# Performance work log

Measured on AMD Instinct MI355X. Metric: run time of the kernel, lower is better.

Reference implementation:

```python
import jax, jax.numpy as jnp
import numpy as np

H = 1024      # hidden_size
I = 2048      # intermediate_size
E = 32        # num_routed_experts
B, S = 4, 2048


def setup_inputs() -> dict:
    key = jax.random.key(0)
    ks = jax.random.split(key, 8)
    scale = 0.02
    inp = {
        "hidden_states": jax.random.normal(ks[0], (B, S, H), dtype=jnp.float32),
        # router gate: stored [H, E] so logits = x @ gate_w
        "gate_w": jax.random.normal(ks[1], (H, E), dtype=jnp.float32) * scale,
        # shared SwiGLU (num_shared_experts=1), weights stored [in, out]
        "shared_gate_w": jax.random.normal(ks[2], (H, I), dtype=jnp.float32) * scale,
        "shared_up_w": jax.random.normal(ks[3], (H, I), dtype=jnp.float32) * scale,
        "shared_down_w": jax.random.normal(ks[4], (I, H), dtype=jnp.float32) * scale,
        # routed grouped SwiGLU, weights stored [E, in, out] (matches GroupedLinear)
        "routed_gate_w": jax.random.normal(ks[5], (E, H, I), dtype=jnp.float32) * scale,
        "routed_up_w": jax.random.normal(ks[6], (E, H, I), dtype=jnp.float32) * scale,
        "routed_down_w": jax.random.normal(ks[7], (E, I, H), dtype=jnp.float32) * scale,
    }
    return inp


def _grouped_mm(a, w, group_sizes):
    # a: [T, in], w: [E, in, out], group_sizes: [E] int32 -> [T, out]
    return jax.lax.ragged_dot(a, w, group_sizes)


def _swiglu(x, gw, uw, dw):
    return (jax.nn.silu(x @ gw) * (x @ uw)) @ dw


def reference(hidden_states, gate_w, shared_gate_w, shared_up_w, shared_down_w,
              routed_gate_w, routed_up_w, routed_down_w):
    b, s, h = hidden_states.shape
    x = hidden_states.reshape(-1, h)                      # [T, H]

    # ---- shared expert ----
    shared_out = _swiglu(x, shared_gate_w, shared_up_w, shared_down_w)

    # ---- router: top-1 ----
    logits = x @ gate_w                                   # [T, E]
    topk_ids = jnp.argmax(logits, axis=-1)                # [T]
    topk_val = jnp.max(logits, axis=-1)                   # [T]
    scores = jax.nn.sigmoid(topk_val)[:, None]            # [T, 1]
    xs = x * scores                                       # scale tokens by router score

    # ---- dispatch: sort tokens by expert id ----
    tokens_per_expert = jnp.zeros((E,), jnp.int32).at[topk_ids].add(1)
    order = jnp.argsort(topk_ids)                         # token ids sorted by expert
    sorted_x = xs[order]                                  # [T, H]

    # ---- grouped SwiGLU experts ----
    g = _grouped_mm(sorted_x, routed_gate_w, tokens_per_expert)   # [T, I]
    u = _grouped_mm(sorted_x, routed_up_w, tokens_per_expert)     # [T, I]
    d = _grouped_mm(jax.nn.silu(g) * u, routed_down_w, tokens_per_expert)  # [T, H]

    # ---- combine: unsort back to token order ----
    inv = jnp.argsort(order)
    routed_out = d[inv]

    return (shared_out + routed_out).reshape(b, s, h)
```

## Files before the change

### kernel.cpp

```cpp
#include <hip/hip_runtime.h>
#include <stdint.h>
#include <stddef.h>

#define TOK 8192
#define H 1024
#define IDIM 2048
#define NE 32
#define BM 128
#define BN 128
#define BK 64
#define MAX_TILES 96

typedef __attribute__((ext_vector_type(8))) short short8;
typedef __attribute__((ext_vector_type(4))) float f32x4;
typedef __attribute__((ext_vector_type(4))) float float4v;
typedef __attribute__((ext_vector_type(4))) unsigned int uint4v;


__device__ __forceinline__ unsigned short f2bf(float x) {
  unsigned u = __builtin_bit_cast(unsigned, x);
  u += 0x7fffu + ((u >> 16) & 1u);
  return (unsigned short)(u >> 16);
}

__device__ __forceinline__ unsigned cvtpk(float lo, float hi) {
  unsigned r;
  asm("v_cvt_pk_bf16_f32 %0, %1, %2" : "=v"(r) : "v"(lo), "v"(hi));
  return r;
}

__device__ __forceinline__ void gll16(const void* g, void* l) {
  __builtin_amdgcn_global_load_lds(
      (const __attribute__((address_space(1))) unsigned int*)g,
      (__attribute__((address_space(3))) unsigned int*)l, 16, 0, 0);
}

__device__ __forceinline__ f32x4 mfma16(short8 a, short8 b, f32x4 c) {
  return __builtin_amdgcn_mfma_f32_16x16x32_bf16(a, b, c, 0, 0, 0);
}

__device__ __forceinline__ int wswz(int n) {
  return ((n ^ (n >> 2)) & 7) << 4;
}


__global__ __launch_bounds__(256) void router_kernel(
    const float* __restrict__ x, const float* __restrict__ gw,
    unsigned short* __restrict__ xbf, unsigned short* __restrict__ xsbf,
    int* __restrict__ expert_id, int* __restrict__ counts)
{
  __shared__ float xl[8 * H];
  __shared__ float plog[8][8][NE];
  __shared__ float sscore[8];
  const int tid = threadIdx.x;
  const long t0 = (long)blockIdx.x * 8;

  const float4v* src = (const float4v*)(x + t0 * H);
  float4v* dst = (float4v*)xl;
  #pragma unroll
  for (int i = 0; i < 8; ++i) dst[tid + i * 256] = src[tid + i * 256];
  __syncthreads();

  {
    const int e = tid & 31, c = tid >> 5;
    float acc[8] = {0, 0, 0, 0, 0, 0, 0, 0};
    const float* gp = gw + (c * 128) * NE + e;
    for (int h = 0; h < 128; ++h) {
      float g = gp[h * NE];
      const float* xr = xl + (c * 128 + h);
      #pragma unroll
      for (int tk = 0; tk < 8; ++tk) acc[tk] += xr[tk * H] * g;
    }
    #pragma unroll
    for (int tk = 0; tk < 8; ++tk) plog[c][tk][e] = acc[tk];
  }
  __syncthreads();
  {
    const int e = tid & 31, tok = tid >> 5;
    float lg = 0.f;
    #pragma unroll
    for (int c = 0; c < 8; ++c) lg += plog[c][tok][e];
    float m = lg; int be = e;
    #pragma unroll
    for (int mask = 16; mask >= 1; mask >>= 1) {
      float om = __shfl_xor(m, mask);
      int   oe = __shfl_xor(be, mask);
      if (om > m || (om == m && oe < be)) { m = om; be = oe; }
    }
    if (e == 0) {
      sscore[tok] = 1.f / (1.f + __expf(-m));
      expert_id[t0 + tok] = be;
      atomicAdd(&counts[be], 1);
    }
  }
  __syncthreads();
  {
    const float sc = sscore[tid >> 5];
    const int base = (tid >> 5) * H + (tid & 31) * 32;
    #pragma unroll
    for (int i = 0; i < 4; ++i) {
      uint4v vx, vs;
      #pragma unroll
      for (int q = 0; q < 4; ++q) {
        const float a = xl[base + i * 8 + 2 * q];
        const float b = xl[base + i * 8 + 2 * q + 1];
        vx[q] = cvtpk(a, b);
        vs[q] = cvtpk(a * sc, b * sc);
      }
      *(uint4v*)(xbf  + t0 * H + base + i * 8) = vx;
      *(uint4v*)(xsbf + t0 * H + base + i * 8) = vs;
    }
  }
}


__global__ void scan_kernel(const int* __restrict__ counts, int* __restrict__ offsets,
                            int* __restrict__ cursor, int* __restrict__ tile_e,
                            int* __restrict__ tile_p, int* __restrict__ n_tiles)
{
  if (threadIdx.x != 0) return;
  int off = 0, nt = 0;
  for (int e = 0; e < NE; ++e) {
    offsets[e] = off; cursor[e] = off;
    int cc = counts[e];
    for (int k = 0; k < cc; k += BM) { tile_e[nt] = e; tile_p[nt] = off + k; ++nt; }
    off += cc;
  }
  offsets[NE] = off;
  n_tiles[0] = nt;
}


__global__ __launch_bounds__(256) void perm_kernel(
    const int* __restrict__ expert_id, int* __restrict__ cursor, int* __restrict__ perm)
{
  int t = blockIdx.x * 256 + threadIdx.x;
  int e = expert_id[t];
  int pos = atomicAdd(&cursor[e], 1);
  perm[pos] = t;
}


template<bool ROUTED>
__global__ __launch_bounds__(256, 2) void gateup_kernel(
    const unsigned short* __restrict__ Abase,
    const float* __restrict__ WgAll, const float* __restrict__ WuAll,
    unsigned short* __restrict__ act,
    const int* __restrict__ perm, const int* __restrict__ tile_e,
    const int* __restrict__ tile_p, const int* __restrict__ offsets,
    const int* __restrict__ n_tiles)
{
  __shared__ short Alds[2][BM * BK];
  __shared__ short Glds[BN * BK];
  __shared__ short Ulds[BN * BK];

  const int tid = threadIdx.x;
  const int wave = tid >> 6, lane = tid & 63;
  const int wm = wave >> 1, wn = wave & 1;

  int row0, row_end;
  const float *Wg, *Wu;
  if constexpr (ROUTED) {
    if ((int)blockIdx.x >= *n_tiles) return;
    const int e = tile_e[blockIdx.x];
    row0 = tile_p[blockIdx.x];
    row_end = offsets[e + 1];
    Wg = WgAll + (size_t)e * H * IDIM;
    Wu = WuAll + (size_t)e * H * IDIM;
  } else {
    row0 = blockIdx.x * BM; row_end = row0 + BM;
    Wg = WgAll; Wu = WuAll;
  }
  const int n0 = blockIdx.y * BN;

  const unsigned short* asrc[4];
  int aoff[4];
  #pragma unroll
  for (int i = 0; i < 4; ++i) {
    const int r = wave * 32 + i * 8 + (lane >> 3);
    int grow;
    if constexpr (ROUTED) {
      int p = row0 + r;
      if (p >= row_end) p = row0;
      grow = perm[p];
    } else grow = row0 + r;
    const int cb = ((lane & 7) * 16) ^ ((r & 7) << 4);
    asrc[i] = Abase + (size_t)grow * H + (cb >> 1);
    aoff[i] = (wave * 32 + i * 8) * BK;
  }

  const int wq = tid >> 5;
  const int wc = tid & 31;

  f32x4 accg[4][4] = {};
  f32x4 accu[4][4] = {};
  float4v g4[8], u4[8];

  auto stageA = [&](int kt) {
    short* base = Alds[kt & 1];
    #pragma unroll
    for (int i = 0; i < 4; ++i) gll16(asrc[i] + kt * BK, base + aoff[i]);
  };
  auto loadW = [&](int kt) {
    const int k0 = kt * BK;
    #pragma unroll
    for (int r = 0; r < 8; ++r) {
      const size_t goff = (size_t)(k0 + wq * 8 + r) * IDIM + (n0 + wc * 4);
      g4[r] = *(const float4v*)(Wg + goff);
      u4[r] = *(const float4v*)(Wu + goff);
    }
  };
  auto writeW = [&]() {
    #pragma unroll
    for (int j = 0; j < 4; ++j) {
      const int n = wc * 4 + j;
      const int cb = (wq * 16) ^ wswz(n);
      uint4v pg, pu;
      pg.x = cvtpk(g4[0][j], g4[1][j]);
      pg.y = cvtpk(g4[2][j], g4[3][j]);
      pg.z = cvtpk(g4[4][j], g4[5][j]);
      pg.w = cvtpk(g4[6][j], g4[7][j]);
      pu.x = cvtpk(u4[0][j], u4[1][j]);
      pu.y = cvtpk(u4[2][j], u4[3][j]);
      pu.z = cvtpk(u4[4][j], u4[5][j]);
      pu.w = cvtpk(u4[6][j], u4[7][j]);
      *(uint4v*)((char*)Glds + n * 128 + cb) = pg;
      *(uint4v*)((char*)Ulds + n * 128 + cb) = pu;
    }
  };
  auto compute = [&](int kt) {
    const char* ab = (const char*)Alds[kt & 1];
    #pragma unroll
    for (int kk = 0; kk < 2; ++kk) {
      short8 af[4];
      #pragma unroll
      for (int m = 0; m < 4; ++m) {
        const int r = wm * 64 + m * 16 + (lane & 15);
        const int cb = (kk * 64 + ((lane >> 4) * 16)) ^ ((r & 7) << 4);
        af[m] = *(const short8*)(ab + r * 128 + cb);
      }
      #pragma unroll
      for (int nf = 0; nf < 4; ++nf) {
        const int n = wn * 64 + nf * 16 + (lane & 15);
        const int cb = (kk * 64 + ((lane >> 4) * 16)) ^ wswz(n);
        short8 bg = *(const short8*)((const char*)Glds + n * 128 + cb);
        short8 bu = *(const short8*)((const char*)Ulds + n * 128 + cb);
        #pragma unroll
        for (int m = 0; m < 4; ++m) {
          accg[m][nf] = mfma16(af[m], bg, accg[m][nf]);
          accu[m][nf] = mfma16(af[m], bu, accu[m][nf]);
        }
      }
    }
  };

  stageA(0);
  loadW(0);
  writeW();
  __syncthreads();

  #pragma unroll 1
  for (int kt = 0; kt < H / BK - 1; ++kt) {
    stageA(kt + 1);
    loadW(kt + 1);
    compute(kt);
    __syncthreads();
    writeW();
    __syncthreads();
  }
  compute(H / BK - 1);

  #pragma unroll
  for (int m = 0; m < 4; ++m)
    #pragma unroll
    for (int nf = 0; nf < 4; ++nf) {
      const int col = n0 + wn * 64 + nf * 16 + (lane & 15);
      #pragma unroll
      for (int j = 0; j < 4; ++j) {
        const int row = row0 + wm * 64 + m * 16 + ((lane >> 4) * 4) + j;
        if (ROUTED && row >= row_end) continue;
        const float g = accg[m][nf][j];
        const float u = accu[m][nf][j];
        const float v = (g / (1.f + __expf(-g))) * u;
        act[(size_t)row * IDIM + col] = f2bf(v);
      }
    }
}


template<bool ROUTED>
__global__ __launch_bounds__(256, 2) void down_kernel(
    const unsigned short* __restrict__ act,
    const float* __restrict__ WdAll,
    float* __restrict__ out,
    const int* __restrict__ perm, const int* __restrict__ tile_e,
    const int* __restrict__ tile_p, const int* __restrict__ offsets,
    const int* __restrict__ n_tiles)
{
  __shared__ short Alds[2][BM * BK];
  __shared__ short Wlds[BN * BK];

  const int tid = threadIdx.x;
  const int wave = tid >> 6, lane = tid & 63;
  const int wm = wave >> 1, wn = wave & 1;

  int row0, row_end;
  const float* Wd;
  if constexpr (ROUTED) {
    if ((int)blockIdx.x >= *n_tiles) return;
    const int e = tile_e[blockIdx.x];
    row0 = tile_p[blockIdx.x];
    row_end = offsets[e + 1];
    Wd = WdAll + (size_t)e * IDIM * H;
  } else {
    row0 = blockIdx.x * BM; row_end = row0 + BM;
    Wd = WdAll;
  }
  const int n0 = blockIdx.y * BN;

  const unsigned short* asrc[4];
  int aoff[4];
  #pragma unroll
  for (int i = 0; i < 4; ++i) {
    const int r = wave * 32 + i * 8 + (lane >> 3);
    int p = row0 + r;
    if (ROUTED && p >= row_end) p = row0;
    const int cb = ((lane & 7) * 16) ^ ((r & 7) << 4);
    asrc[i] = act + (size_t)p * IDIM + (cb >> 1);
    aoff[i] = (wave * 32 + i * 8) * BK;
  }

  const int wq = tid >> 5;
  const int wc = tid & 31;

  f32x4 acc[4][4] = {};
  float4v w4[8];

  auto stageA = [&](int kt) {
    short* base = Alds[kt & 1];
    #pragma unroll
    for (int i = 0; i < 4; ++i) gll16(asrc[i] + kt * BK, base + aoff[i]);
  };
  auto loadW = [&](int kt) {
    const int k0 = kt * BK;
    #pragma unroll
    for (int r = 0; r < 8; ++r)
      w4[r] = *(const float4v*)(Wd + (size_t)(k0 + wq * 8 + r) * H + (n0 + wc * 4));
  };
  auto writeW = [&]() {
    #pragma unroll
    for (int j = 0; j < 4; ++j) {
      const int n = wc * 4 + j;
      const int cb = (wq * 16) ^ wswz(n);
      uint4v pw;
      pw.x = cvtpk(w4[0][j], w4[1][j]);
      pw.y = cvtpk(w4[2][j], w4[3][j]);
      pw.z = cvtpk(w4[4][j], w4[5][j]);
      pw.w = cvtpk(w4[6][j], w4[7][j]);
      *(uint4v*)((char*)Wlds + n * 128 + cb) = pw;
    }
  };
  auto compute = [&](int kt) {
    const char* ab = (const char*)Alds[kt & 1];
    #pragma unroll
    for (int kk = 0; kk < 2; ++kk) {
      short8 af[4];
      #pragma unroll
      for (int m = 0; m < 4; ++m) {
        const int r = wm * 64 + m * 16 + (lane & 15);
        const int cb = (kk * 64 + ((lane >> 4) * 16)) ^ ((r & 7) << 4);
        af[m] = *(const short8*)(ab + r * 128 + cb);
      }
      #pragma unroll
      for (int nf = 0; nf < 4; ++nf) {
        const int n = wn * 64 + nf * 16 + (lane & 15);
        const int cb = (kk * 64 + ((lane >> 4) * 16)) ^ wswz(n);
        short8 bw = *(const short8*)((const char*)Wlds + n * 128 + cb);
        #pragma unroll
        for (int m = 0; m < 4; ++m) acc[m][nf] = mfma16(af[m], bw, acc[m][nf]);
      }
    }
  };

  stageA(0);
  loadW(0);
  writeW();
  __syncthreads();

  #pragma unroll 1
  for (int kt = 0; kt < IDIM / BK - 1; ++kt) {
    stageA(kt + 1);
    loadW(kt + 1);
    compute(kt);
    __syncthreads();
    writeW();
    __syncthreads();
  }
  compute(IDIM / BK - 1);

  #pragma unroll
  for (int m = 0; m < 4; ++m)
    #pragma unroll
    for (int nf = 0; nf < 4; ++nf) {
      const int col = n0 + wn * 64 + nf * 16 + (lane & 15);
      #pragma unroll
      for (int j = 0; j < 4; ++j) {
        const int row = row0 + wm * 64 + m * 16 + ((lane >> 4) * 4) + j;
        const float v = acc[m][nf][j];
        if constexpr (ROUTED) {
          if (row < row_end) {
            const int t = perm[row];
            out[(size_t)t * H + col] += v;
          }
        } else {
          out[(size_t)row * H + col] = v;
        }
      }
    }
}


extern "C" void kernel_launch(void* const* d_in, const int* in_sizes, int n_in,
                              void* d_out, int out_size, void* d_ws, size_t ws_size,
                              hipStream_t stream) {
  (void)in_sizes; (void)n_in; (void)out_size; (void)ws_size;
  const float* x      = (const float*)d_in[0];
  const float* gate_w = (const float*)d_in[1];
  const float* sgw    = (const float*)d_in[2];
  const float* suw    = (const float*)d_in[3];
  const float* sdw    = (const float*)d_in[4];
  const float* rgw    = (const float*)d_in[5];
  const float* ruw    = (const float*)d_in[6];
  const float* rdw    = (const float*)d_in[7];
  float* out = (float*)d_out;

  char* ws = (char*)d_ws;
  unsigned short* xbf  = (unsigned short*)(ws + 0);
  unsigned short* xsbf = (unsigned short*)(ws + 16777216);
  unsigned short* act  = (unsigned short*)(ws + 33554432);
  int* perm      = (int*)(ws + 67108864);
  int* expert_id = (int*)(ws + 67141632);
  int* counts    = (int*)(ws + 67174400);
  int* offsets   = (int*)(ws + 67174528);
  int* cursor    = (int*)(ws + 67174784);
  int* tile_e    = (int*)(ws + 67174912);
  int* tile_p    = (int*)(ws + 67175424);
  int* n_tiles   = (int*)(ws + 67175936);

  hipMemsetAsync(counts, 0, NE * sizeof(int), stream);
  router_kernel<<<TOK / 8, 256, 0, stream>>>(x, gate_w, xbf, xsbf, expert_id, counts);
  scan_kernel<<<1, 64, 0, stream>>>(counts, offsets, cursor, tile_e, tile_p, n_tiles);
  perm_kernel<<<TOK / 256, 256, 0, stream>>>(expert_id, cursor, perm);

  gateup_kernel<false><<<dim3(TOK / BM, IDIM / BN), 256, 0, stream>>>(
      xbf, sgw, suw, act, perm, tile_e, tile_p, offsets, n_tiles);
  down_kernel<false><<<dim3(TOK / BM, H / BN), 256, 0, stream>>>(
      act, sdw, out, perm, tile_e, tile_p, offsets, n_tiles);
  gateup_kernel<true><<<dim3(MAX_TILES, IDIM / BN), 256, 0, stream>>>(
      xsbf, rgw, ruw, act, perm, tile_e, tile_p, offsets, n_tiles);
  down_kernel<true><<<dim3(MAX_TILES, H / BN), 256, 0, stream>>>(
      act, rdw, out, perm, tile_e, tile_p, offsets, n_tiles);
}
```

Baseline: 648.0 us.

## Halve N tile to 64 and raise occupancy in gate-up and down kernels

Shrinks the output tile width from 128 to 64 columns, with each wave now covering 32 rows by all 64 columns. Thread-to-weight load and LDS write mappings are adjusted to match, and launch bounds rise to 3 and 4 blocks per CU. The aim is to cut accumulator registers and LDS per block so more blocks run concurrently and the grid is larger, which helps the ragged routed tiles fill the GPU. The cost is that each A tile is re-read for twice as many column blocks, and there is less MFMA reuse per weight load.

```diff
diff --git a/kernel.cpp b/kernel.cpp
--- a/kernel.cpp
+++ b/kernel.cpp
@@ -7,13 +7,14 @@
 #define IDIM 2048
 #define NE 32
 #define BM 128
-#define BN 128
+#define BN 64
 #define BK 64
 #define MAX_TILES 96
 
 typedef __attribute__((ext_vector_type(8))) short short8;
 typedef __attribute__((ext_vector_type(4))) float f32x4;
 typedef __attribute__((ext_vector_type(4))) float float4v;
+typedef __attribute__((ext_vector_type(2))) unsigned int uint2v;
 typedef __attribute__((ext_vector_type(4))) unsigned int uint4v;
 
 
@@ -142,7 +143,7 @@
 
 
 template<bool ROUTED>
-__global__ __launch_bounds__(256, 2) void gateup_kernel(
+__global__ __launch_bounds__(256, 3) void gateup_kernel(
     const unsigned short* __restrict__ Abase,
     const float* __restrict__ WgAll, const float* __restrict__ WuAll,
     unsigned short* __restrict__ act,
@@ -156,7 +157,6 @@
 
   const int tid = threadIdx.x;
   const int wave = tid >> 6, lane = tid & 63;
-  const int wm = wave >> 1, wn = wave & 1;
 
   int row0, row_end;
   const float *Wg, *Wu;
@@ -189,12 +189,12 @@
     aoff[i] = (wave * 32 + i * 8) * BK;
   }
 
-  const int wq = tid >> 5;
-  const int wc = tid & 31;
-
-  f32x4 accg[4][4] = {};
-  f32x4 accu[4][4] = {};
-  float4v g4[8], u4[8];
+  const int wq = tid >> 4;
+  const int wc = tid & 15;
+
+  f32x4 accg[2][4] = {};
+  f32x4 accu[2][4] = {};
+  float4v g4[4], u4[4];
 
   auto stageA = [&](int kt) {
     short* base = Alds[kt & 1];
@@ -204,8 +204,8 @@
   auto loadW = [&](int kt) {
     const int k0 = kt * BK;
     #pragma unroll
-    for (int r = 0; r < 8; ++r) {
-      const size_t goff = (size_t)(k0 + wq * 8 + r) * IDIM + (n0 + wc * 4);
+    for (int r = 0; r < 4; ++r) {
+      const size_t goff = (size_t)(k0 + wq * 4 + r) * IDIM + (n0 + wc * 4);
       g4[r] = *(const float4v*)(Wg + goff);
       u4[r] = *(const float4v*)(Wu + goff);
     }
@@ -214,39 +214,35 @@
     #pragma unroll
     for (int j = 0; j < 4; ++j) {
       const int n = wc * 4 + j;
-      const int cb = (wq * 16) ^ wswz(n);
-      uint4v pg, pu;
+      const int cb = (wq * 8) ^ wswz(n);
+      uint2v pg, pu;
       pg.x = cvtpk(g4[0][j], g4[1][j]);
       pg.y = cvtpk(g4[2][j], g4[3][j]);
-      pg.z = cvtpk(g4[4][j], g4[5][j]);
-      pg.w = cvtpk(g4[6][j], g4[7][j]);
       pu.x = cvtpk(u4[0][j], u4[1][j]);
       pu.y = cvtpk(u4[2][j], u4[3][j]);
-      pu.z = cvtpk(u4[4][j], u4[5][j]);
-      pu.w = cvtpk(u4[6][j], u4[7][j]);
-      *(uint4v*)((char*)Glds + n * 128 + cb) = pg;
-      *(uint4v*)((char*)Ulds + n * 128 + cb) = pu;
+      *(uint2v*)((char*)Glds + n * 128 + cb) = pg;
+      *(uint2v*)((char*)Ulds + n * 128 + cb) = pu;
     }
   };
   auto compute = [&](int kt) {
     const char* ab = (const char*)Alds[kt & 1];
     #pragma unroll
     for (int kk = 0; kk < 2; ++kk) {
-      short8 af[4];
-      #pragma unroll
-      for (int m = 0; m < 4; ++m) {
-        const int r = wm * 64 + m * 16 + (lane & 15);
+      short8 af[2];
+      #pragma unroll
+      for (int m = 0; m < 2; ++m) {
+        const int r = wave * 32 + m * 16 + (lane & 15);
         const int cb = (kk * 64 + ((lane >> 4) * 16)) ^ ((r & 7) << 4);
         af[m] = *(const short8*)(ab + r * 128 + cb);
       }
       #pragma unroll
       for (int nf = 0; nf < 4; ++nf) {
-        const int n = wn * 64 + nf * 16 + (lane & 15);
+        const int n = nf * 16 + (lane & 15);
         const int cb = (kk * 64 + ((lane >> 4) * 16)) ^ wswz(n);
         short8 bg = *(const short8*)((const char*)Glds + n * 128 + cb);
         short8 bu = *(const short8*)((const char*)Ulds + n * 128 + cb);
         #pragma unroll
-        for (int m = 0; m < 4; ++m) {
+        for (int m = 0; m < 2; ++m) {
           accg[m][nf] = mfma16(af[m], bg, accg[m][nf]);
           accu[m][nf] = mfma16(af[m], bu, accu[m][nf]);
         }
@@ -271,13 +267,13 @@
   compute(H / BK - 1);
 
   #pragma unroll
-  for (int m = 0; m < 4; ++m)
+  for (int m = 0; m < 2; ++m)
     #pragma unroll
     for (int nf = 0; nf < 4; ++nf) {
-      const int col = n0 + wn * 64 + nf * 16 + (lane & 15);
+      const int col = n0 + nf * 16 + (lane & 15);
       #pragma unroll
       for (int j = 0; j < 4; ++j) {
-        const int row = row0 + wm * 64 + m * 16 + ((lane >> 4) * 4) + j;
+        const int row = row0 + wave * 32 + m * 16 + ((lane >> 4) * 4) + j;
         if (ROUTED && row >= row_end) continue;
         const float g = accg[m][nf][j];
         const float u = accu[m][nf][j];
@@ -289,7 +285,7 @@
 
 
 template<bool ROUTED>
-__global__ __launch_bounds__(256, 2) void down_kernel(
+__global__ __launch_bounds__(256, 4) void down_kernel(
     const unsigned short* __restrict__ act,
     const float* __restrict__ WdAll,
     float* __restrict__ out,
@@ -302,7 +298,6 @@
 
   const int tid = threadIdx.x;
   const int wave = tid >> 6, lane = tid & 63;
-  const int wm = wave >> 1, wn = wave & 1;
 
   int row0, row_end;
   const float* Wd;
@@ -330,11 +325,11 @@
     aoff[i] = (wave * 32 + i * 8) * BK;
   }
 
-  const int wq = tid >> 5;
-  const int wc = tid & 31;
-
-  f32x4 acc[4][4] = {};
-  float4v w4[8];
+  const int wq = tid >> 4;
+  const int wc = tid & 15;
+
+  f32x4 acc[2][4] = {};
+  float4v w4[4];
 
   auto stageA = [&](int kt) {
     short* base = Alds[kt & 1];
@@ -344,40 +339,38 @@
   auto loadW = [&](int kt) {
     const int k0 = kt * BK;
     #pragma unroll
-    for (int r = 0; r < 8; ++r)
-      w4[r] = *(const float4v*)(Wd + (size_t)(k0 + wq * 8 + r) * H + (n0 + wc * 4));
+    for (int r = 0; r < 4; ++r)
+      w4[r] = *(const float4v*)(Wd + (size_t)(k0 + wq * 4 + r) * H + (n0 + wc * 4));
   };
   auto writeW = [&]() {
     #pragma unroll
     for (int j = 0; j < 4; ++j) {
       const int n = wc * 4 + j;
-      const int cb = (wq * 16) ^ wswz(n);
-      uint4v pw;
+      const int cb = (wq * 8) ^ wswz(n);
+      uint2v pw;
       pw.x = cvtpk(w4[0][j], w4[1][j]);
       pw.y = cvtpk(w4[2][j], w4[3][j]);
-      pw.z = cvtpk(w4[4][j], w4[5][j]);
-      pw.w = cvtpk(w4[6][j], w4[7][j]);
-      *(uint4v*)((char*)Wlds + n * 128 + cb) = pw;
+      *(uint2v*)((char*)Wlds + n * 128 + cb) = pw;
     }
   };
   auto compute = [&](int kt) {
     const char* ab = (const char*)Alds[kt & 1];
     #pragma unroll
     for (int kk = 0; kk < 2; ++kk) {
-      short8 af[4];
-      #pragma unroll
-      for (int m = 0; m < 4; ++m) {
-        const int r = wm * 64 + m * 16 + (lane & 15);
+      short8 af[2];
+      #pragma unroll
+      for (int m = 0; m < 2; ++m) {
+        const int r = wave * 32 + m * 16 + (lane & 15);
         const int cb = (kk * 64 + ((lane >> 4) * 16)) ^ ((r & 7) << 4);
         af[m] = *(const short8*)(ab + r * 128 + cb);
       }
       #pragma unroll
       for (int nf = 0; nf < 4; ++nf) {
-        const int n = wn * 64 + nf * 16 + (lane & 15);
+        const int n = nf * 16 + (lane & 15);
         const int cb = (kk * 64 + ((lane >> 4) * 16)) ^ wswz(n);
         short8 bw = *(const short8*)((const char*)Wlds + n * 128 + cb);
         #pragma unroll
-        for (int m = 0; m < 4; ++m) acc[m][nf] = mfma16(af[m], bw, acc[m][nf]);
+        for (int m = 0; m < 2; ++m) acc[m][nf] = mfma16(af[m], bw, acc[m][nf]);
       }
     }
   };
@@ -399,13 +392,13 @@
   compute(IDIM / BK - 1);
 
   #pragma unroll
-  for (int m = 0; m < 4; ++m)
+  for (int m = 0; m < 2; ++m)
     #pragma unroll
     for (int nf = 0; nf < 4; ++nf) {
-      const int col = n0 + wn * 64 + nf * 16 + (lane & 15);
+      const int col = n0 + nf * 16 + (lane & 15);
       #pragma unroll
       for (int j = 0; j < 4; ++j) {
-        const int row = row0 + wm * 64 + m * 16 + ((lane >> 4) * 4) + j;
+        const int row = row0 + wave * 32 + m * 16 + ((lane >> 4) * 4) + j;
         const float v = acc[m][nf][j];
         if constexpr (ROUTED) {
           if (row < row_end) {
```

After: 661.0 us. About the same (+2.0%).

## Pre-transpose weights to bf16 and load all GEMM operands directly into LDS

Applied to the files above, without the earlier changes.

Adds a transpose-and-convert kernel that writes every fp32 weight matrix into a K-contiguous bf16 copy in workspace on each call. The gate/up and down GEMMs then stream both A and the weights into LDS with global_load_lds, dropping the per-tile register load, fp32 to bf16 conversion and swizzled LDS write of the weights. This trades a full extra pass over all weights against cheaper, half-width weight rereads in the GEMMs. The K loop also drops the double-buffered A staging for a single buffer with two barriers per step, and the down kernel asks for higher occupancy.

```diff
diff --git a/kernel.cpp b/kernel.cpp
--- a/kernel.cpp
+++ b/kernel.cpp
@@ -7,7 +7,6 @@
 #define IDIM 2048
 #define NE 32
 #define BM 128
-#define BN 128
 #define BK 64
 #define MAX_TILES 96
 
@@ -39,8 +38,43 @@
   return __builtin_amdgcn_mfma_f32_16x16x32_bf16(a, b, c, 0, 0, 0);
 }
 
-__device__ __forceinline__ int wswz(int n) {
-  return ((n ^ (n >> 2)) & 7) << 4;
+
+__global__ __launch_bounds__(256) void tconv_kernel(
+    const float* __restrict__ src0, unsigned short* __restrict__ dst0,
+    int K, int N)
+{
+  __shared__ float t[64][65];
+  const size_t mat = (size_t)K * N;
+  const float* src = src0 + (size_t)blockIdx.z * mat;
+  unsigned short* dst = dst0 + (size_t)blockIdx.z * mat;
+  const int k0 = blockIdx.x * 64, n0 = blockIdx.y * 64;
+  const int tid = threadIdx.x;
+  {
+    const int r = tid >> 4;
+    const int c = (tid & 15) * 4;
+    #pragma unroll
+    for (int i = 0; i < 4; ++i) {
+      float4v v = *(const float4v*)(src + (size_t)(k0 + r + i * 16) * N + (n0 + c));
+      t[r + i * 16][c + 0] = v[0];
+      t[r + i * 16][c + 1] = v[1];
+      t[r + i * 16][c + 2] = v[2];
+      t[r + i * 16][c + 3] = v[3];
+    }
+  }
+  __syncthreads();
+  {
+    const int n = tid >> 2;
+    const int kc = (tid & 3) * 16;
+    uint4v o0, o1;
+    #pragma unroll
+    for (int q = 0; q < 4; ++q) {
+      o0[q] = cvtpk(t[kc + 2 * q][n],     t[kc + 2 * q + 1][n]);
+      o1[q] = cvtpk(t[kc + 8 + 2 * q][n], t[kc + 8 + 2 * q + 1][n]);
+    }
+    unsigned short* dp = dst + (size_t)(n0 + n) * K + (k0 + kc);
+    *(uint4v*)dp = o0;
+    *(uint4v*)(dp + 8) = o1;
+  }
 }
 
 
@@ -142,94 +176,68 @@
 
 
 template<bool ROUTED>
-__global__ __launch_bounds__(256, 2) void gateup_kernel(
-    const unsigned short* __restrict__ Abase,
-    const float* __restrict__ WgAll, const float* __restrict__ WuAll,
+__global__ __launch_bounds__(256, 2) void gu_kernel(
+    const unsigned short* __restrict__ A,
+    const unsigned short* __restrict__ GT,
+    const unsigned short* __restrict__ UT,
     unsigned short* __restrict__ act,
     const int* __restrict__ perm, const int* __restrict__ tile_e,
     const int* __restrict__ tile_p, const int* __restrict__ offsets,
     const int* __restrict__ n_tiles)
 {
-  __shared__ short Alds[2][BM * BK];
-  __shared__ short Glds[BN * BK];
-  __shared__ short Ulds[BN * BK];
+  __shared__ short Al[BM * BK];
+  __shared__ short Gl[128 * BK];
+  __shared__ short Ul[128 * BK];
 
   const int tid = threadIdx.x;
   const int wave = tid >> 6, lane = tid & 63;
   const int wm = wave >> 1, wn = wave & 1;
 
   int row0, row_end;
-  const float *Wg, *Wu;
+  const unsigned short *Gt, *Ut;
   if constexpr (ROUTED) {
     if ((int)blockIdx.x >= *n_tiles) return;
     const int e = tile_e[blockIdx.x];
     row0 = tile_p[blockIdx.x];
     row_end = offsets[e + 1];
-    Wg = WgAll + (size_t)e * H * IDIM;
-    Wu = WuAll + (size_t)e * H * IDIM;
+    Gt = GT + (size_t)e * H * IDIM;
+    Ut = UT + (size_t)e * H * IDIM;
   } else {
     row0 = blockIdx.x * BM; row_end = row0 + BM;
-    Wg = WgAll; Wu = WuAll;
-  }
-  const int n0 = blockIdx.y * BN;
-
-  const unsigned short* asrc[4];
-  int aoff[4];
+    Gt = GT; Ut = UT;
+  }
+  const int n0 = blockIdx.y * 128;
+
+  const unsigned short *asrc[4], *gsrc[4], *usrc[4];
+  int soff[4];
   #pragma unroll
   for (int i = 0; i < 4; ++i) {
     const int r = wave * 32 + i * 8 + (lane >> 3);
-    int grow;
-    if constexpr (ROUTED) {
-      int p = row0 + r;
-      if (p >= row_end) p = row0;
-      grow = perm[p];
-    } else grow = row0 + r;
+    int p = row0 + r;
+    if (ROUTED && p >= row_end) p = row0;
+    int arow = p;
+    if constexpr (ROUTED) arow = perm[p];
     const int cb = ((lane & 7) * 16) ^ ((r & 7) << 4);
-    asrc[i] = Abase + (size_t)grow * H + (cb >> 1);
-    aoff[i] = (wave * 32 + i * 8) * BK;
-  }
-
-  const int wq = tid >> 5;
-  const int wc = tid & 31;
+    asrc[i] = A  + (size_t)arow * H + (cb >> 1);
+    gsrc[i] = Gt + (size_t)(n0 + r) * H + (cb >> 1);
+    usrc[i] = Ut + (size_t)(n0 + r) * H + (cb >> 1);
+    soff[i] = (wave * 32 + i * 8) * BK;
+  }
 
   f32x4 accg[4][4] = {};
   f32x4 accu[4][4] = {};
-  float4v g4[8], u4[8];
-
-  auto stageA = [&](int kt) {
-    short* base = Alds[kt & 1];
-    #pragma unroll
-    for (int i = 0; i < 4; ++i) gll16(asrc[i] + kt * BK, base + aoff[i]);
-  };
-  auto loadW = [&](int kt) {
-    const int k0 = kt * BK;
-    #pragma unroll
-    for (int r = 0; r < 8; ++r) {
-      const size_t goff = (size_t)(k0 + wq * 8 + r) * IDIM + (n0 + wc * 4);
-      g4[r] = *(const float4v*)(Wg + goff);
-      u4[r] = *(const float4v*)(Wu + goff);
-    }
-  };
-  auto writeW = [&]() {
-    #pragma unroll
-    for (int j = 0; j < 4; ++j) {
-      const int n = wc * 4 + j;
-      const int cb = (wq * 16) ^ wswz(n);
-      uint4v pg, pu;
-      pg.x = cvtpk(g4[0][j], g4[1][j]);
-      pg.y = cvtpk(g4[2][j], g4[3][j]);
-      pg.z = cvtpk(g4[4][j], g4[5][j]);
-      pg.w = cvtpk(g4[6][j], g4[7][j]);
-      pu.x = cvtpk(u4[0][j], u4[1][j]);
-      pu.y = cvtpk(u4[2][j], u4[3][j]);
-      pu.z = cvtpk(u4[4][j], u4[5][j]);
-      pu.w = cvtpk(u4[6][j], u4[7][j]);
-      *(uint4v*)((char*)Glds + n * 128 + cb) = pg;
-      *(uint4v*)((char*)Ulds + n * 128 + cb) = pu;
-    }
-  };
-  auto compute = [&](int kt) {
-    const char* ab = (const char*)Alds[kt & 1];
+
+  #pragma unroll 1
+  for (int kt = 0; kt < H / BK; ++kt) {
+    __syncthreads();
+    #pragma unroll
+    for (int i = 0; i < 4; ++i) gll16(asrc[i] + kt * BK, Al + soff[i]);
+    #pragma unroll
+    for (int i = 0; i < 4; ++i) gll16(gsrc[i] + kt * BK, Gl + soff[i]);
+    #pragma unroll
+    for (int i = 0; i < 4; ++i) gll16(usrc[i] + kt * BK, Ul + soff[i]);
+    __syncthreads();
+
     #pragma unroll
     for (int kk = 0; kk < 2; ++kk) {
       short8 af[4];
@@ -237,14 +245,14 @@
       for (int m = 0; m < 4; ++m) {
         const int r = wm * 64 + m * 16 + (lane & 15);
         const int cb = (kk * 64 + ((lane >> 4) * 16)) ^ ((r & 7) << 4);
-        af[m] = *(const short8*)(ab + r * 128 + cb);
+        af[m] = *(const short8*)((const char*)Al + r * 128 + cb);
       }
       #pragma unroll
       for (int nf = 0; nf < 4; ++nf) {
         const int n = wn * 64 + nf * 16 + (lane & 15);
-        const int cb = (kk * 64 + ((lane >> 4) * 16)) ^ wswz(n);
-        short8 bg = *(const short8*)((const char*)Glds + n * 128 + cb);
-        short8 bu = *(const short8*)((const char*)Ulds + n * 128 + cb);
+        const int cb = (kk * 64 + ((lane >> 4) * 16)) ^ ((n & 7) << 4);
+        short8 bg = *(const short8*)((const char*)Gl + n * 128 + cb);
+        short8 bu = *(const short8*)((const char*)Ul + n * 128 + cb);
         #pragma unroll
         for (int m = 0; m < 4; ++m) {
           accg[m][nf] = mfma16(af[m], bg, accg[m][nf]);
@@ -252,23 +260,7 @@
         }
       }
     }
-  };
-
-  stageA(0);
-  loadW(0);
-  writeW();
-  __syncthreads();
-
-  #pragma unroll 1
-  for (int kt = 0; kt < H / BK - 1; ++kt) {
-    stageA(kt + 1);
-    loadW(kt + 1);
-    compute(kt);
-    __syncthreads();
-    writeW();
-    __syncthreads();
-  }
-  compute(H / BK - 1);
+  }
 
   #pragma unroll
   for (int m = 0; m < 4; ++m)
@@ -289,79 +281,59 @@
 
 
 template<bool ROUTED>
-__global__ __launch_bounds__(256, 2) void down_kernel(
-    const unsigned short* __restrict__ act,
-    const float* __restrict__ WdAll,
+__global__ __launch_bounds__(256, 4) void dn_kernel(
+    const unsigned short* __restrict__ A,
+    const unsigned short* __restrict__ DT,
     float* __restrict__ out,
     const int* __restrict__ perm, const int* __restrict__ tile_e,
     const int* __restrict__ tile_p, const int* __restrict__ offsets,
     const int* __restrict__ n_tiles)
 {
-  __shared__ short Alds[2][BM * BK];
-  __shared__ short Wlds[BN * BK];
+  __shared__ short Al[BM * BK];
+  __shared__ short Dl[128 * BK];
 
   const int tid = threadIdx.x;
   const int wave = tid >> 6, lane = tid & 63;
   const int wm = wave >> 1, wn = wave & 1;
 
   int row0, row_end;
-  const float* Wd;
+  const unsigned short* Dt;
   if constexpr (ROUTED) {
     if ((int)blockIdx.x >= *n_tiles) return;
     const int e = tile_e[blockIdx.x];
     row0 = tile_p[blockIdx.x];
     row_end = offsets[e + 1];
-    Wd = WdAll + (size_t)e * IDIM * H;
+    Dt = DT + (size_t)e * H * IDIM;
   } else {
     row0 = blockIdx.x * BM; row_end = row0 + BM;
-    Wd = WdAll;
-  }
-  const int n0 = blockIdx.y * BN;
-
-  const unsigned short* asrc[4];
-  int aoff[4];
+    Dt = DT;
+  }
+  const int n0 = blockIdx.y * 128;
+
+  const unsigned short *asrc[4], *dsrc[4];
+  int soff[4];
   #pragma unroll
   for (int i = 0; i < 4; ++i) {
     const int r = wave * 32 + i * 8 + (lane >> 3);
     int p = row0 + r;
     if (ROUTED && p >= row_end) p = row0;
     const int cb = ((lane & 7) * 16) ^ ((r & 7) << 4);
-    asrc[i] = act + (size_t)p * IDIM + (cb >> 1);
-    aoff[i] = (wave * 32 + i * 8) * BK;
-  }
-
-  const int wq = tid >> 5;
-  const int wc = tid & 31;
+    asrc[i] = A  + (size_t)p * IDIM + (cb >> 1);
+    dsrc[i] = Dt + (size_t)(n0 + r) * IDIM + (cb >> 1);
+    soff[i] = (wave * 32 + i * 8) * BK;
+  }
 
   f32x4 acc[4][4] = {};
-  float4v w4[8];
-
-  auto stageA = [&](int kt) {
-    short* base = Alds[kt & 1];
-    #pragma unroll
-    for (int i = 0; i < 4; ++i) gll16(asrc[i] + kt * BK, base + aoff[i]);
-  };
-  auto loadW = [&](int kt) {
-    const int k0 = kt * BK;
-    #pragma unroll
-    for (int r = 0; r < 8; ++r)
-      w4[r] = *(const float4v*)(Wd + (size_t)(k0 + wq * 8 + r) * H + (n0 + wc * 4));
-  };
-  auto writeW = [&]() {
-    #pragma unroll
-    for (int j = 0; j < 4; ++j) {
-      const int n = wc * 4 + j;
-      const int cb = (wq * 16) ^ wswz(n);
-      uint4v pw;
-      pw.x = cvtpk(w4[0][j], w4[1][j]);
-      pw.y = cvtpk(w4[2][j], w4[3][j]);
-      pw.z = cvtpk(w4[4][j], w4[5][j]);
-      pw.w = cvtpk(w4[6][j], w4[7][j]);
-      *(uint4v*)((char*)Wlds + n * 128 + cb) = pw;
-    }
-  };
-  auto compute = [&](int kt) {
-    const char* ab = (const char*)Alds[kt & 1];
+
+  #pragma unroll 1
+  for (int kt = 0; kt < IDIM / BK; ++kt) {
+    __syncthreads();
+    #pragma unroll
+    for (int i = 0; i < 4; ++i) gll16(asrc[i] + kt * BK, Al + soff[i]);
+    #pragma unroll
+    for (int i = 0; i < 4; ++i) gll16(dsrc[i] + kt * BK, Dl + soff[i]);
+    __syncthreads();
+
     #pragma unroll
     for (int kk = 0; kk < 2; ++kk) {
       short8 af[4];
@@ -369,34 +341,18 @@
       for (int m = 0; m < 4; ++m) {
         const int r = wm * 64 + m * 16 + (lane & 15);
         const int cb = (kk * 64 + ((lane >> 4) * 16)) ^ ((r & 7) << 4);
-        af[m] = *(const short8*)(ab + r * 128 + cb);
+        af[m] = *(const short8*)((const char*)Al + r * 128 + cb);
       }
       #pragma unroll
       for (int nf = 0; nf < 4; ++nf) {
         const int n = wn * 64 + nf * 16 + (lane & 15);
-        const int cb = (kk * 64 + ((lane >> 4) * 16)) ^ wswz(n);
-        short8 bw = *(const short8*)((const char*)Wlds + n * 128 + cb);
+        const int cb = (kk * 64 + ((lane >> 4) * 16)) ^ ((n & 7) << 4);
+        short8 bd = *(const short8*)((const char*)Dl + n * 128 + cb);
         #pragma unroll
-        for (int m = 0; m < 4; ++m) acc[m][nf] = mfma16(af[m], bw, acc[m][nf]);
-      }
-    }
-  };
-
-  stageA(0);
-  loadW(0);
-  writeW();
-  __syncthreads();
-
-  #pragma unroll 1
-  for (int kt = 0; kt < IDIM / BK - 1; ++kt) {
-    stageA(kt + 1);
-    loadW(kt + 1);
-    compute(kt);
-    __syncthreads();
-    writeW();
-    __syncthreads();
-  }
-  compute(IDIM / BK - 1);
+        for (int m = 0; m < 4; ++m) acc[m][nf] = mfma16(af[m], bd, acc[m][nf]);
+      }
+    }
+  }
 
   #pragma unroll
   for (int m = 0; m < 4; ++m)
@@ -446,18 +402,33 @@
   int* tile_e    = (int*)(ws + 67174912);
   int* tile_p    = (int*)(ws + 67175424);
   int* n_tiles   = (int*)(ws + 67175936);
+  unsigned short* rgwT = (unsigned short*)(ws + 68157440);
+  unsigned short* ruwT = (unsigned short*)(ws + 202375168);
+  unsigned short* rdwT = (unsigned short*)(ws + 336592896);
+  unsigned short* sgwT = (unsigned short*)(ws + 470810624);
+  unsigned short* suwT = (unsigned short*)(ws + 475004928);
+  unsigned short* sdwT = (unsigned short*)(ws + 479199232);
 
   hipMemsetAsync(counts, 0, NE * sizeof(int), stream);
+
+  tconv_kernel<<<dim3(H / 64, IDIM / 64, NE), 256, 0, stream>>>(rgw, rgwT, H, IDIM);
+  tconv_kernel<<<dim3(H / 64, IDIM / 64, NE), 256, 0, stream>>>(ruw, ruwT, H, IDIM);
+  tconv_kernel<<<dim3(IDIM / 64, H / 64, NE), 256, 0, stream>>>(rdw, rdwT, IDIM, H);
+  tconv_kernel<<<dim3(H / 64, IDIM / 64, 1), 256, 0, stream>>>(sgw, sgwT, H, IDIM);
+  tconv_kernel<<<dim3(H / 64, IDIM / 64, 1), 256, 0, stream>>>(suw, suwT, H, IDIM);
+  tconv_kernel<<<dim3(IDIM / 64, H / 64, 1), 256, 0, stream>>>(sdw, sdwT, IDIM, H);
+
   router_kernel<<<TOK / 8, 256, 0, stream>>>(x, gate_w, xbf, xsbf, expert_id, counts);
   scan_kernel<<<1, 64, 0, stream>>>(counts, offsets, cursor, tile_e, tile_p, n_tiles);
   perm_kernel<<<TOK / 256, 256, 0, stream>>>(expert_id, cursor, perm);
 
-  gateup_kernel<false><<<dim3(TOK / BM, IDIM / BN), 256, 0, stream>>>(
-      xbf, sgw, suw, act, perm, tile_e, tile_p, offsets, n_tiles);
-  down_kernel<false><<<dim3(TOK / BM, H / BN), 256, 0, stream>>>(
-      act, sdw, out, perm, tile_e, tile_p, offsets, n_tiles);
-  gateup_kernel<true><<<dim3(MAX_TILES, IDIM / BN), 256, 0, stream>>>(
-      xsbf, rgw, ruw, act, perm, tile_e, tile_p, offsets, n_tiles);
-  down_kernel<true><<<dim3(MAX_TILES, H / BN), 256, 0, stream>>>(
-      act, rdw, out, perm, tile_e, tile_p, offsets, n_tiles);
-}
+  gu_kernel<false><<<dim3(TOK / BM, IDIM / 128), 256, 0, stream>>>(
+      xbf, sgwT, suwT, act, perm, tile_e, tile_p, offsets, n_tiles);
+  dn_kernel<false><<<dim3(TOK / BM, H / 128), 256, 0, stream>>>(
+      act, sdwT, out, perm, tile_e, tile_p, offsets, n_tiles);
+
+  gu_kernel<true><<<dim3(MAX_TILES, IDIM / 128), 256, 0, stream>>>(
+      xsbf, rgwT, ruwT, act, perm, tile_e, tile_p, offsets, n_tiles);
+  dn_kernel<true><<<dim3(MAX_TILES, H / 128), 256, 0, stream>>>(
+      act, rdwT, out, perm, tile_e, tile_p, offsets, n_tiles);
+}
```

After: 647.0 us. Within noise of the previous version (-0.2%).
